# Optimization experiments

Hardware: AMD Instinct MI355X
Metric: run time of the kernel (lower is better)

## Reference

```python
import jax, jax.numpy as jnp
import numpy as np

VOCAB, EMB, HID, OUT_VOCAB, LAYERS = 256, 512, 1024, 256, 2
B, T = 128, 512
LN_EPS = 1e-5


def _run_layer(seq_tbi, Wi, bi, Wh):
    # seq_tbi: [T, B, in_dim]; Wi: [H, in_dim]; bi: [H]; Wh: [H, H]
    h0 = jnp.zeros((seq_tbi.shape[1], Wh.shape[0]), dtype=seq_tbi.dtype)
    xproj = jnp.einsum('tbi,hi->tbh', seq_tbi, Wi) + bi  # precompute input projection

    def step(h, xp_t):
        h_new = jnp.tanh(xp_t + h @ Wh.T)
        return h_new, h_new

    _, hs = jax.lax.scan(step, h0, xproj)  # hs: [T, B, H]
    return hs


def setup_inputs() -> dict:
    key = jax.random.key(0)
    ks = jax.random.split(key, 10)

    def xavier(k, shape):
        fan_in, fan_out = shape[1], shape[0]
        lim = np.sqrt(6.0 / (fan_in + fan_out))
        return jax.random.uniform(k, shape, jnp.float32, -lim, lim)

    def ortho(k, n):
        a = jax.random.normal(k, (n, n), jnp.float32)
        q, r = jnp.linalg.qr(a)
        return q * jnp.sign(jnp.diag(r))[None, :]

    emb = xavier(ks[0], (VOCAB, EMB))
    wi0 = xavier(ks[1], (HID, EMB))
    bi0 = jnp.zeros((HID,), jnp.float32)
    wh0 = ortho(ks[2], HID)
    wi1 = xavier(ks[3], (HID, HID))
    bi1 = jnp.zeros((HID,), jnp.float32)
    wh1 = ortho(ks[4], HID)
    ln_g = jnp.ones((HID,), jnp.float32)
    ln_b = jnp.zeros((HID,), jnp.float32)
    proj_w = xavier(ks[5], (OUT_VOCAB, HID))
    proj_b = jnp.zeros((OUT_VOCAB,), jnp.float32)
    x = jax.random.randint(ks[6], (B, T), 0, VOCAB)
    return {"emb": emb, "wi0": wi0, "bi0": bi0, "wh0": wh0,
            "wi1": wi1, "bi1": bi1, "wh1": wh1,
            "ln_g": ln_g, "ln_b": ln_b, "proj_w": proj_w, "proj_b": proj_b,
            "x": x}


def reference(emb, wi0, bi0, wh0, wi1, bi1, wh1, ln_g, ln_b, proj_w, proj_b, x):
    # x: [B, T] int -> embeddings [T, B, E] (time-major for scan)
    embs = emb[x].transpose(1, 0, 2)
    hs = _run_layer(embs, wi0, bi0, wh0)      # [T, B, H]
    hs = _run_layer(hs, wi1, bi1, wh1)        # [T, B, H]
    # LayerNorm over last dim, then projection, vectorized over all steps
    mu = hs.mean(-1, keepdims=True)
    var = ((hs - mu) ** 2).mean(-1, keepdims=True)
    normed = (hs - mu) * jax.lax.rsqrt(var + LN_EPS) * ln_g + ln_b
    logits = jnp.einsum('tbh,vh->tbv', normed, proj_w) + proj_b
    return logits.transpose(1, 0, 2)  # [B, T, OUT_VOCAB]
```

## Files before the change

### kernel.cpp

```cpp
#include <hip/hip_runtime.h>
#include <hip/hip_bf16.h>


typedef __bf16 bf16;
typedef _Float16 f16;
typedef _Float16 f16x8 __attribute__((ext_vector_type(8)));
typedef float f32x4 __attribute__((ext_vector_type(4)));
typedef unsigned long long u64;

#define TSTEPS 512
#define BATCH  128
#define HID    1024
#define NST    515
#define FAST_SPIN_MAX 64

__device__ __forceinline__ f32x4 mfma16(f16x8 a, f16x8 b, f32x4 c) {
    return __builtin_amdgcn_mfma_f32_16x16x32_f16(a, b, c, 0, 0, 0);
}

__device__ __forceinline__ f16x8 lda16(const f16* p) {
    union { u64 u[2]; f16x8 v; } c;
    c.u[0] = __hip_atomic_load((const u64*)p,     __ATOMIC_RELAXED, __HIP_MEMORY_SCOPE_AGENT);
    c.u[1] = __hip_atomic_load((const u64*)p + 1, __ATOMIC_RELAXED, __HIP_MEMORY_SCOPE_AGENT);
    return c.v;
}
__device__ __forceinline__ void sth2(f16* p, f16 v) {
    union { f16 f; unsigned short s; } c; c.f = v;
    __hip_atomic_store((unsigned short*)p, c.s, __ATOMIC_RELAXED, __HIP_MEMORY_SCOPE_AGENT);
}
__device__ __forceinline__ void stf4(float* p, float v) {
    union { float f; unsigned u; } c; c.f = v;
    __hip_atomic_store((unsigned*)p, c.u, __ATOMIC_RELAXED, __HIP_MEMORY_SCOPE_AGENT);
}
__device__ __forceinline__ float ldf4c(const float* p) {
    union { float f; unsigned u; } c;
    c.u = __hip_atomic_load((const unsigned*)p, __ATOMIC_RELAXED, __HIP_MEMORY_SCOPE_AGENT);
    return c.f;
}

__device__ __forceinline__ unsigned f16bits32(f16 v) {
    union { f16 f; unsigned short s; } c; c.f = v; return (unsigned)c.s;
}

__device__ __forceinline__ float ldf(const void* p, size_t i, bool f32) {
    return f32 ? ((const float*)p)[i] : (float)((const bf16*)p)[i];
}

__global__ void det_kernel(const unsigned short* __restrict__ e, unsigned* __restrict__ flag) {
    int tid = threadIdx.x;
    int cnt = 0;
    for (int i = tid; i < 1024; i += 256) {
        unsigned short u = e[i];
        int ex = (u >> 7) & 0xFF;
        if ((ex >= 110 && ex <= 131) || u == 0) cnt++;
    }
    __shared__ int sh[256];
    sh[tid] = cnt; __syncthreads();
    for (int s = 128; s > 0; s >>= 1) { if (tid < s) sh[tid] += sh[tid + s]; __syncthreads(); }
    if (tid == 0) *flag = (sh[0] >= 768) ? 0u : 1u;
}

__global__ void etab_kernel(const void* __restrict__ emb, const void* __restrict__ wi0,
                            const void* __restrict__ bi0, const unsigned* __restrict__ flag,
                            float* __restrict__ etab) {
    const bool f32 = (*flag != 0);
    int i = blockIdx.x * 256 + threadIdx.x;
    int v = i >> 10, ch = i & 1023;
    float s = ldf(bi0, ch, f32);
    for (int e = 0; e < 512; ++e)
        s += ldf(emb, (size_t)v * 512 + e, f32) * ldf(wi0, (size_t)ch * 512 + e, f32);
    etab[i] = s;
}

__global__ void c12_kernel(const void* __restrict__ pw, const void* __restrict__ g,
                           const void* __restrict__ be, const void* __restrict__ pb,
                           const unsigned* __restrict__ flag, float* __restrict__ c12) {
    const bool f32 = (*flag != 0);
    int v = threadIdx.x;
    float a = 0.f, b = 0.f;
    for (int k = 0; k < 1024; ++k) {
        float w = ldf(pw, (size_t)v * 1024 + k, f32);
        a += (float)(f16)(w * ldf(g, k, f32));
        b += w * ldf(be, k, f32);
    }
    c12[v] = a;
    c12[256 + v] = b + ldf(pb, v, f32);
}

template<bool FAST>
__device__ __forceinline__ void run_loop(
    const int role, const int rid, const int gbase,
    const int tid, const int lane, const int n, const int quad,
    const int ch, const int outv,
    const f16x8 (&wf)[32], const float bias, const float c1v, const float c2v,
    const bool f32io,
    const float* __restrict__ etab, const int* __restrict__ x,
    f16* __restrict__ h0buf, f16* __restrict__ h1buf, float* __restrict__ xpf,
    void* __restrict__ out, unsigned* __restrict__ myc,
    f16 (&As)[16][1032])
{
    for (int t = 0; t < NST; ++t) {
        bool active;
        f16* rbuf;
        if (role == 0)      { active = (t < 512);            rbuf = h0buf; }
        else if (role == 1) { active = (t >= 1 && t <= 512); rbuf = h0buf; }
        else if (role == 2) { active = (t >= 2 && t <= 513); rbuf = h1buf; }
        else                { active = (t >= 3 && t <= 514); rbuf = h1buf; }

        if (active) {
            const f16* Abase = rbuf + ((t + 1) & 1) * (BATCH * HID)
                             + (size_t)gbase * HID;

            float ev[4] = {0.f, 0.f, 0.f, 0.f};
            if (role == 0) {
#pragma unroll
                for (int r = 0; r < 4; ++r) {
                    int b = gbase + quad * 4 + r;
                    ev[r] = etab[(size_t)x[b * TSTEPS + t] * HID + ch];
                }
            } else if (role == 2) {
                const float* xs = xpf + (t & 1) * (BATCH * HID);
                if constexpr (FAST) {
                    const float* p0 = xs + (size_t)(gbase + quad * 4 + 0) * HID + ch;
                    const float* p1 = xs + (size_t)(gbase + quad * 4 + 1) * HID + ch;
                    const float* p2 = xs + (size_t)(gbase + quad * 4 + 2) * HID + ch;
                    const float* p3 = xs + (size_t)(gbase + quad * 4 + 3) * HID + ch;
                    asm volatile(
                        "global_load_dword %0, %4, off sc0\n\t"
                        "global_load_dword %1, %5, off sc0\n\t"
                        "global_load_dword %2, %6, off sc0\n\t"
                        "global_load_dword %3, %7, off sc0\n\t"
                        "s_waitcnt vmcnt(0)"
                        : "=&v"(ev[0]), "=&v"(ev[1]), "=&v"(ev[2]), "=&v"(ev[3])
                        : "v"(p0), "v"(p1), "v"(p2), "v"(p3)
                        : "memory");
                } else {
#pragma unroll
                    for (int r = 0; r < 4; ++r)
                        ev[r] = ldf4c(xs + (size_t)(gbase + quad * 4 + r) * HID + ch);
                }
            }

            if constexpr (FAST) {
                const f16* ga[4]; f16* da[4];
#pragma unroll
                for (int it = 0; it < 4; ++it) {
                    int idx = it * 512 + tid;
                    int row = idx >> 7, col = (idx & 127) << 3;
                    ga[it] = Abase + (size_t)row * HID + col;
                    da[it] = &As[row][col];
                }
                f32x4 v0, v1, v2, v3;
                asm volatile(
                    "global_load_dwordx4 %0, %4, off sc0\n\t"
                    "global_load_dwordx4 %1, %5, off sc0\n\t"
                    "global_load_dwordx4 %2, %6, off sc0\n\t"
                    "global_load_dwordx4 %3, %7, off sc0\n\t"
                    "s_waitcnt vmcnt(0)"
                    : "=&v"(v0), "=&v"(v1), "=&v"(v2), "=&v"(v3)
                    : "v"(ga[0]), "v"(ga[1]), "v"(ga[2]), "v"(ga[3])
                    : "memory");
                *(f32x4*)da[0] = v0;
                *(f32x4*)da[1] = v1;
                *(f32x4*)da[2] = v2;
                *(f32x4*)da[3] = v3;
            } else {
#pragma unroll
                for (int it = 0; it < 4; ++it) {
                    int idx = it * 512 + tid;
                    int row = idx >> 7, col = (idx & 127) << 3;
                    f16x8 v = lda16(Abase + (size_t)row * HID + col);
                    *(f16x8*)&As[row][col] = v;
                }
            }

            __syncthreads();

            float mu = 0.f, rs = 0.f;
            if (role == 3) {
                const f16* srow = &As[n][quad * 256];
                float sum = 0.f, sq = 0.f;
#pragma unroll
                for (int i = 0; i < 256; i += 8) {
                    f16x8 hv = *(const f16x8*)(srow + i);
#pragma unroll
                    for (int j = 0; j < 8; ++j) {
                        float e = (float)hv[j];
                        sum += e; sq += e * e;
                    }
                }
                sum += __shfl_xor(sum, 16); sq += __shfl_xor(sq, 16);
                sum += __shfl_xor(sum, 32); sq += __shfl_xor(sq, 32);
                mu = sum * (1.f / 1024.f);
                float var = sq * (1.f / 1024.f) - mu * mu;
                rs = rsqrtf(fmaxf(var, 0.f) + 1e-5f);
            }

            const f16* arow = &As[n][quad * 8];
            f32x4 a0 = {0,0,0,0}, a1 = {0,0,0,0}, a2 = {0,0,0,0}, a3 = {0,0,0,0};
#pragma unroll
            for (int kt = 0; kt < 32; kt += 4) {
                a0 = mfma16(*(const f16x8*)(arow + (kt + 0) * 32), wf[kt + 0], a0);
                a1 = mfma16(*(const f16x8*)(arow + (kt + 1) * 32), wf[kt + 1], a1);
                a2 = mfma16(*(const f16x8*)(arow + (kt + 2) * 32), wf[kt + 2], a2);
                a3 = mfma16(*(const f16x8*)(arow + (kt + 3) * 32), wf[kt + 3], a3);
            }
            f32x4 acc = (a0 + a1) + (a2 + a3);

            if (role == 0 || role == 2) {
                f16* dw = ((role == 0) ? h0buf : h1buf) + (t & 1) * (BATCH * HID);
                if constexpr (FAST) {
                    unsigned u0 = f16bits32((f16)tanhf(acc[0] + ev[0]));
                    unsigned u1 = f16bits32((f16)tanhf(acc[1] + ev[1]));
                    unsigned u2 = f16bits32((f16)tanhf(acc[2] + ev[2]));
                    unsigned u3 = f16bits32((f16)tanhf(acc[3] + ev[3]));
                    f16* q0 = dw + (size_t)(gbase + quad * 4 + 0) * HID + ch;
                    f16* q1 = dw + (size_t)(gbase + quad * 4 + 1) * HID + ch;
                    f16* q2 = dw + (size_t)(gbase + quad * 4 + 2) * HID + ch;
                    f16* q3 = dw + (size_t)(gbase + quad * 4 + 3) * HID + ch;
                    asm volatile(
                        "global_store_short %4, %0, off sc0\n\t"
                        "global_store_short %5, %1, off sc0\n\t"
                        "global_store_short %6, %2, off sc0\n\t"
                        "global_store_short %7, %3, off sc0\n\t"
                        "s_waitcnt vmcnt(0)"
                        :: "v"(u0), "v"(u1), "v"(u2), "v"(u3),
                           "v"(q0), "v"(q1), "v"(q2), "v"(q3)
                        : "memory");
                } else {
#pragma unroll
                    for (int r = 0; r < 4; ++r) {
                        int b = gbase + quad * 4 + r;
                        sth2(dw + (size_t)b * HID + ch, (f16)tanhf(acc[r] + ev[r]));
                    }
                }
            } else if (role == 1) {
                float* dw = xpf + ((t + 1) & 1) * (BATCH * HID);
                if constexpr (FAST) {
                    float w0 = acc[0] + bias, w1 = acc[1] + bias;
                    float w2 = acc[2] + bias, w3 = acc[3] + bias;
                    float* q0 = dw + (size_t)(gbase + quad * 4 + 0) * HID + ch;
                    float* q1 = dw + (size_t)(gbase + quad * 4 + 1) * HID + ch;
                    float* q2 = dw + (size_t)(gbase + quad * 4 + 2) * HID + ch;
                    float* q3 = dw + (size_t)(gbase + quad * 4 + 3) * HID + ch;
                    asm volatile(
                        "global_store_dword %4, %0, off sc0\n\t"
                        "global_store_dword %5, %1, off sc0\n\t"
                        "global_store_dword %6, %2, off sc0\n\t"
                        "global_store_dword %7, %3, off sc0\n\t"
                        "s_waitcnt vmcnt(0)"
                        :: "v"(w0), "v"(w1), "v"(w2), "v"(w3),
                           "v"(q0), "v"(q1), "v"(q2), "v"(q3)
                        : "memory");
                } else {
#pragma unroll
                    for (int r = 0; r < 4; ++r) {
                        int b = gbase + quad * 4 + r;
                        stf4(dw + (size_t)b * HID + ch, acc[r] + bias);
                    }
                }
            } else {
                int s = t - 3;
#pragma unroll
                for (int r = 0; r < 4; ++r) {
                    int m = quad * 4 + r;
                    float mm = __shfl(mu, m), rr = __shfl(rs, m);
                    float lv = rr * acc[r] - rr * mm * c1v + c2v;
                    size_t oi = ((size_t)(gbase + m) * TSTEPS + s) * 256 + outv;
                    if (f32io) ((float*)out)[oi] = lv;
                    else       ((bf16*)out)[oi]  = (bf16)lv;
                }
            }
        }

        __syncthreads();
        if constexpr (FAST) {
            const unsigned want = (unsigned)(t + 1);
            if (tid < 64) {
                if (lane == 0) {
                    unsigned* ms = myc + rid;
                    asm volatile(
                        "global_store_dword %0, %1, off sc0\n\t"
                        "s_waitcnt vmcnt(0)"
                        :: "v"(ms), "v"(want) : "memory");
                }
                const unsigned* sp = myc + lane;
                bool done = false;
                for (int it = 0; it < FAST_SPIN_MAX; ++it) {
                    unsigned v = (lane < 26)
                        ? __hip_atomic_load(sp, __ATOMIC_RELAXED, __HIP_MEMORY_SCOPE_AGENT)
                        : want;
                    if (__all(v >= want)) { done = true; break; }
                    __builtin_amdgcn_s_sleep(1);
                }
                if (lane == 0)
                    __hip_atomic_fetch_add(myc + 31, 1u, __ATOMIC_RELAXED,
                                           __HIP_MEMORY_SCOPE_AGENT);
                if (!done && lane == 0) {
                    const unsigned tgt = 26u * want;
                    while (__hip_atomic_load(myc + 31, __ATOMIC_RELAXED,
                                             __HIP_MEMORY_SCOPE_AGENT) < tgt)
                        __builtin_amdgcn_s_sleep(1);
                }
            }
        } else {
            if (tid == 0) {
                __hip_atomic_fetch_add(myc, 1u, __ATOMIC_RELAXED, __HIP_MEMORY_SCOPE_AGENT);
                const unsigned tgt = 26u * (unsigned)(t + 1);
                while (__hip_atomic_load(myc, __ATOMIC_RELAXED, __HIP_MEMORY_SCOPE_AGENT) < tgt)
                    __builtin_amdgcn_s_sleep(1);
            }
        }
        __syncthreads();
    }
}

__global__ __launch_bounds__(512, 2) void mega_kernel(
    const void* __restrict__ wh0, const void* __restrict__ wi1,
    const void* __restrict__ wh1, const void* __restrict__ pw,
    const void* __restrict__ lng, const void* __restrict__ bi1,
    const float* __restrict__ etab, const float* __restrict__ c12,
    const int* __restrict__ x, const unsigned* __restrict__ flag,
    f16* __restrict__ h0buf, f16* __restrict__ h1buf, float* __restrict__ xpf,
    void* __restrict__ out, unsigned* __restrict__ cnt)
{
    const bool f32io = (*flag != 0);
    const int bid  = blockIdx.x;
    const int g    = bid & 7, rid = bid >> 3;
    const int role = rid >> 3;
    const int slice = rid & 7;
    const int tid  = threadIdx.x;
    const int wave = tid >> 6, lane = tid & 63;
    const int n    = lane & 15, quad = lane >> 4;
    const int gbase = g * 16;
    unsigned* const myc = cnt + g * 32;

    __shared__ __align__(16) f16 As[16][1032];

    f16x8 wf[32];
    float bias = 0.f, c1v = 0.f, c2v = 0.f;
    int ch = 0, outv = 0;
    if (role < 3) {
        ch = slice * 128 + wave * 16 + n;
        const void* W = (role == 0) ? wh0 : ((role == 1) ? wi1 : wh1);
#pragma unroll
        for (int kt = 0; kt < 32; ++kt) {
            f16x8 t;
#pragma unroll
            for (int j = 0; j < 8; ++j)
                t[j] = (f16)ldf(W, (size_t)ch * HID + kt * 32 + quad * 8 + j, f32io);
            wf[kt] = t;
        }
        if (role == 1) bias = ldf(bi1, ch, f32io);
    } else {
        int tile = slice * 8 + wave;
        outv = tile * 16 + n;
#pragma unroll
        for (int kt = 0; kt < 32; ++kt) {
            f16x8 t;
#pragma unroll
            for (int j = 0; j < 8; ++j) {
                int k = kt * 32 + quad * 8 + j;
                t[j] = (f16)(ldf(pw, (size_t)outv * HID + k, f32io) * ldf(lng, k, f32io));
            }
            wf[kt] = t;
        }
        c1v = c12[outv];
        c2v = c12[256 + outv];
    }

    unsigned xcc = 0;
    asm volatile("s_getreg_b32 %0, hwreg(HW_REG_XCC_ID)" : "=s"(xcc));
    xcc &= 0xFu;
    __shared__ int fsh;
    if (tid == 0) {
        const unsigned my = 0x100u | xcc;
        __hip_atomic_store(cnt + 256 + bid, my, __ATOMIC_RELAXED, __HIP_MEMORY_SCOPE_AGENT);
        int ok = 1;
        for (int r = 0; r < 26; ++r) {
            unsigned v;
            for (;;) {
                v = __hip_atomic_load(cnt + 256 + g + 8 * r, __ATOMIC_RELAXED, __HIP_MEMORY_SCOPE_AGENT);
                if (v & 0x100u) break;
                __builtin_amdgcn_s_sleep(2);
            }
            if (v != my) ok = 0;
        }
        fsh = ok;
    }
    __syncthreads();
    const bool fast = (fsh != 0);

    if (fast)
        run_loop<true >(role, rid, gbase, tid, lane, n, quad, ch, outv, wf, bias, c1v, c2v,
                        f32io, etab, x, h0buf, h1buf, xpf, out, myc, As);
    else
        run_loop<false>(role, rid, gbase, tid, lane, n, quad, ch, outv, wf, bias, c1v, c2v,
                        f32io, etab, x, h0buf, h1buf, xpf, out, myc, As);
}

extern "C" void kernel_launch(void* const* d_in, const int* in_sizes, int n_in,
                              void* d_out, int out_size, void* d_ws, size_t ws_size,
                              hipStream_t stream) {
    const void* emb    = d_in[0];
    const void* wi0    = d_in[1];
    const void* bi0    = d_in[2];
    const void* wh0    = d_in[3];
    const void* wi1    = d_in[4];
    const void* bi1    = d_in[5];
    const void* wh1    = d_in[6];
    const void* ln_g   = d_in[7];
    const void* ln_b   = d_in[8];
    const void* proj_w = d_in[9];
    const void* proj_b = d_in[10];
    const int*  x      = (const int*)d_in[11];
    char* ws = (char*)d_ws;

    float*    etab  = (float*)(ws + 0);
    float*    c12   = (float*)(ws + 1048576);
    unsigned* flag  = (unsigned*)(ws + 1050624);
    f16*      h0buf = (f16*)(ws + 1050688);
    f16*      h1buf = (f16*)(ws + 1574976);
    float*    xpf   = (float*)(ws + 2099264);
    unsigned* cnt   = (unsigned*)(ws + 3147840);
    if (ws_size < 3151936u) return;

    hipMemsetAsync(ws + 1050624, 0, 3151936 - 1050624, stream);

    det_kernel<<<1, 256, 0, stream>>>((const unsigned short*)emb, flag);
    etab_kernel<<<1024, 256, 0, stream>>>(emb, wi0, bi0, flag, etab);
    c12_kernel<<<1, 256, 0, stream>>>(proj_w, ln_g, ln_b, proj_b, flag, c12);
    mega_kernel<<<208, 512, 0, stream>>>(wh0, wi1, wh1, proj_w, ln_g, bi1,
                                         etab, c12, x, flag,
                                         h0buf, h1buf, xpf, d_out, cnt);
}
```

Before: 3.361 ms.

## Replace global barrier with role-specific dependency waits on producer flags

Each block now polls only the per-block step flags of the roles it actually depends on, instead of waiting for all 26 blocks and falling back to a shared atomic counter. The s_waitcnt after the flag store and after the xproj loads is also removed. The goal is to cut barrier latency and atomic contention on the serial recurrence path. It risks memory-ordering races: dropping the wait after the flag store could publish the flag before the data is visible, and the dependency masks must exactly match the data flow.

Result: faster. 3.161 ms (-5.9%).

```diff
diff --git a/kernel.cpp b/kernel.cpp
--- a/kernel.cpp
+++ b/kernel.cpp
@@ -12,7 +12,6 @@
 #define BATCH  128
 #define HID    1024
 #define NST    515
-#define FAST_SPIN_MAX 64
 
 __device__ __forceinline__ f32x4 mfma16(f16x8 a, f16x8 b, f32x4 c) {
     return __builtin_amdgcn_mfma_f32_16x16x32_f16(a, b, c, 0, 0, 0);
@@ -99,6 +98,12 @@
     void* __restrict__ out, unsigned* __restrict__ myc,
     f16 (&As)[16][1032])
 {
+    bool need = false;
+    if (role == 0)      need = (lane < 16) && (lane != rid);
+    else if (role == 1) need = (lane < 8) || (lane >= 16 && lane < 24);
+    else if (role == 2) need = (lane >= 8 && lane < 26) && (lane != rid);
+    else                need = (lane >= 16 && lane < 24);
+
     for (int t = 0; t < NST; ++t) {
         bool active;
         f16* rbuf;
@@ -129,8 +134,7 @@
                         "global_load_dword %0, %4, off sc0\n\t"
                         "global_load_dword %1, %5, off sc0\n\t"
                         "global_load_dword %2, %6, off sc0\n\t"
-                        "global_load_dword %3, %7, off sc0\n\t"
-                        "s_waitcnt vmcnt(0)"
+                        "global_load_dword %3, %7, off sc0"
                         : "=&v"(ev[0]), "=&v"(ev[1]), "=&v"(ev[2]), "=&v"(ev[3])
                         : "v"(p0), "v"(p1), "v"(p2), "v"(p3)
                         : "memory");
@@ -279,28 +283,16 @@
             if (tid < 64) {
                 if (lane == 0) {
                     unsigned* ms = myc + rid;
-                    asm volatile(
-                        "global_store_dword %0, %1, off sc0\n\t"
-                        "s_waitcnt vmcnt(0)"
-                        :: "v"(ms), "v"(want) : "memory");
-                }
-                const unsigned* sp = myc + lane;
-                bool done = false;
-                for (int it = 0; it < FAST_SPIN_MAX; ++it) {
-                    unsigned v = (lane < 26)
-                        ? __hip_atomic_load(sp, __ATOMIC_RELAXED, __HIP_MEMORY_SCOPE_AGENT)
-                        : want;
-                    if (__all(v >= want)) { done = true; break; }
+                    asm volatile("global_store_dword %0, %1, off sc0"
+                                 :: "v"(ms), "v"(want) : "memory");
+                }
+                for (;;) {
+                    unsigned v = want;
+                    if (need)
+                        v = __hip_atomic_load(myc + lane, __ATOMIC_RELAXED,
+                                              __HIP_MEMORY_SCOPE_AGENT);
+                    if (__all(v >= want)) break;
                     __builtin_amdgcn_s_sleep(1);
-                }
-                if (lane == 0)
-                    __hip_atomic_fetch_add(myc + 31, 1u, __ATOMIC_RELAXED,
-                                           __HIP_MEMORY_SCOPE_AGENT);
-                if (!done && lane == 0) {
-                    const unsigned tgt = 26u * want;
-                    while (__hip_atomic_load(myc + 31, __ATOMIC_RELAXED,
-                                             __HIP_MEMORY_SCOPE_AGENT) < tgt)
-                        __builtin_amdgcn_s_sleep(1);
                 }
             }
         } else {
```
